# Kernel optimization log

Hardware: AMD Instinct MI355X
Metric: run time of the kernel (lower is better)

Reference implementation:

```python
import jax, jax.numpy as jnp
import numpy as np

NUM_GROUPS = 8
K = 2


def setup_inputs() -> dict:
    key = jax.random.key(0)
    k1, k2, k3 = jax.random.split(key, 3)
    b, l, d = 4, 4096, 2048
    g, k = NUM_GROUPS, K
    hdg = d // g  # 256
    x = jax.random.normal(k1, (b, l, d), dtype=jnp.float32)
    Wg = jax.random.normal(k2, (d, g), dtype=jnp.float32) * 0.02  # gate (no bias)
    Wm = jax.random.normal(k3, (k * hdg, k * hdg), dtype=jnp.float32) * 0.02  # inner Linear
    bm = jnp.zeros((k * hdg,), dtype=jnp.float32)
    return {"x": x, "Wg": Wg, "Wm": Wm, "bm": bm}


def reference(x, Wg, Wm, bm):
    b, l, d = x.shape
    g, k = NUM_GROUPS, K
    hdg = d // g
    # gate: softmax + topk over groups
    S = jax.nn.softmax(x @ Wg, axis=-1)            # [b, l, g]
    G, I = jax.lax.top_k(S, k)                     # [b, l, k] each
    x4 = x.reshape(b, l, g, hdg)
    # gather selected feature groups
    sel = jnp.take_along_axis(x4, I[..., None], axis=2)  # [b, l, k, hdg]
    h = (G[..., None] * sel).reshape(b, l, k * hdg)
    # inner model (Linear)
    h = h @ Wm + bm
    h = h.reshape(b, l, k, hdg)
    # scatter back into original groups
    bi = jnp.arange(b)[:, None, None]
    li = jnp.arange(l)[None, :, None]
    out = x4.at[bi, li, I].set(h)
    return out.reshape(b, l, d)
```

## Files before the change

kernel.cpp:

```cpp
#include <hip/hip_runtime.h>
#include <hip/hip_bf16.h>

#define NTOK   16384
#define DIM    2048
#define NGRP   8
#define HDG    256
#define NIN    512

typedef float f32x4 __attribute__((ext_vector_type(4)));
typedef short bf16x8 __attribute__((ext_vector_type(8)));

static __device__ __forceinline__ unsigned short f2bf(float f) {
    unsigned int u = __builtin_bit_cast(unsigned int, f);
    u = (u + 0x7fffu + ((u >> 16) & 1u)) >> 16;
    return (unsigned short)u;
}

__global__ __launch_bounds__(256) void prep_wm(const float* __restrict__ Wm,
                                               ushort* __restrict__ WmT) {
    __shared__ float tile[64][65];
    const int bk = blockIdx.x * 64;
    const int bn = blockIdx.y * 64;
    const int t = threadIdx.x;
    const int r = t >> 4;
    const int c = (t & 15) * 4;
#pragma unroll
    for (int i = 0; i < 4; i++) {
        const float4 v = *(const float4*)&Wm[(bk + r + i * 16) * 512 + bn + c];
        tile[r + i * 16][c + 0] = v.x;
        tile[r + i * 16][c + 1] = v.y;
        tile[r + i * 16][c + 2] = v.z;
        tile[r + i * 16][c + 3] = v.w;
    }
    __syncthreads();
#pragma unroll
    for (int i = 0; i < 4; i++) {
        const int n = r + i * 16;
        ushort4 o;
        o.x = f2bf(tile[c + 0][n]);
        o.y = f2bf(tile[c + 1][n]);
        o.z = f2bf(tile[c + 2][n]);
        o.w = f2bf(tile[c + 3][n]);
        *(ushort4*)&WmT[(bn + n) * 512 + bk + c] = o;
    }
}

__global__ __launch_bounds__(256) void gate_gather(
        const float* __restrict__ x, const float* __restrict__ Wg,
        float* __restrict__ out, ushort* __restrict__ hbuf,
        int* __restrict__ Isel) {
    const int t = threadIdx.x;
    const int lane = t & 63;
    const int wave = t >> 6;
    float wgr[8][8];
#pragma unroll
    for (int j = 0; j < 8; j++) {
        const float4 a = *(const float4*)&Wg[(t * 8 + j) * 8];
        const float4 b = *(const float4*)&Wg[(t * 8 + j) * 8 + 4];
        wgr[j][0] = a.x; wgr[j][1] = a.y; wgr[j][2] = a.z; wgr[j][3] = a.w;
        wgr[j][4] = b.x; wgr[j][5] = b.y; wgr[j][6] = b.z; wgr[j][7] = b.w;
    }
    __shared__ float red[8][4][8];
    const int tok0 = blockIdx.x * 8;

    const bool b0 = lane & 1;
    const bool b1 = lane & 2;
    const bool b2 = lane & 4;

#pragma unroll
    for (int tt = 0; tt < 8; tt++) {
        const int tok = tok0 + tt;
        const float4 x0 = *(const float4*)&x[tok * DIM + t * 8];
        const float4 x1 = *(const float4*)&x[tok * DIM + t * 8 + 4];
        const float xr[8] = {x0.x, x0.y, x0.z, x0.w, x1.x, x1.y, x1.z, x1.w};
        float acc[8];
#pragma unroll
        for (int g = 0; g < 8; g++) acc[g] = 0.f;
#pragma unroll
        for (int j = 0; j < 8; j++)
#pragma unroll
            for (int g = 0; g < 8; g++)
                acc[g] = fmaf(xr[j], wgr[j][g], acc[g]);
        float n_[4];
#pragma unroll
        for (int j = 0; j < 4; j++) {
            const float keep = b0 ? acc[2 * j + 1] : acc[2 * j];
            const float send = b0 ? acc[2 * j] : acc[2 * j + 1];
            n_[j] = keep + __shfl_xor(send, 1, 64);
        }
        float m_[2];
#pragma unroll
        for (int j = 0; j < 2; j++) {
            const float keep = b1 ? n_[2 * j + 1] : n_[2 * j];
            const float send = b1 ? n_[2 * j] : n_[2 * j + 1];
            m_[j] = keep + __shfl_xor(send, 2, 64);
        }
        float v;
        {
            const float keep = b2 ? m_[1] : m_[0];
            const float send = b2 ? m_[0] : m_[1];
            v = keep + __shfl_xor(send, 4, 64);
        }
        v += __shfl_xor(v, 8, 64);
        v += __shfl_xor(v, 16, 64);
        v += __shfl_xor(v, 32, 64);
        if (lane < 8) red[tt][wave][lane] = v;
    }
    __syncthreads();

    const int ll = lane & 31;
    const int tok_local = wave * 2 + (lane >> 5);
    const int tok = tok0 + tok_local;

    float v = red[tok_local][ll >> 3][ll & 7];
    v += __shfl_xor(v, 8, 64);
    v += __shfl_xor(v, 16, 64);
    float c[8];
    c[0] = v;
    c[1] = __shfl_xor(c[0], 1, 64);
    c[2] = __shfl_xor(c[0], 2, 64);
    c[3] = __shfl_xor(c[1], 2, 64);
    c[4] = __shfl_xor(c[0], 4, 64);
    c[5] = __shfl_xor(c[1], 4, 64);
    c[6] = __shfl_xor(c[2], 4, 64);
    c[7] = __shfl_xor(c[3], 4, 64);
    const int gbase = ll & 7;

    float m = c[0];
#pragma unroll
    for (int j = 1; j < 8; j++) m = fmaxf(m, c[j]);
    float sum = 0.f;
#pragma unroll
    for (int j = 0; j < 8; j++) sum += __expf(c[j] - m);
    int i0 = 8; float v0 = -3.4e38f;
#pragma unroll
    for (int j = 0; j < 8; j++) {
        const int g = gbase ^ j;
        if (c[j] > v0 || (c[j] == v0 && g < i0)) { v0 = c[j]; i0 = g; }
    }
    int i1 = 8; float v1 = -3.4e38f;
#pragma unroll
    for (int j = 0; j < 8; j++) {
        const int g = gbase ^ j;
        if (g != i0 && (c[j] > v1 || (c[j] == v1 && g < i1))) { v1 = c[j]; i1 = g; }
    }
    const float inv = 1.0f / sum;
    const float G0 = __expf(v0 - m) * inv;
    const float G1 = __expf(v1 - m) * inv;

#pragma unroll
    for (int cgrp = 0; cgrp < 8; cgrp++) {
        const float4 f0 = *(const float4*)&x[tok * DIM + cgrp * HDG + ll * 8];
        const float4 f1 = *(const float4*)&x[tok * DIM + cgrp * HDG + ll * 8 + 4];
        if (cgrp == i0 || cgrp == i1) {
            const float gv  = (cgrp == i0) ? G0 : G1;
            const int slot  = (cgrp == i0) ? 0 : 1;
            int4 pk;
            pk.x = (int)f2bf(gv * f0.x) | ((int)f2bf(gv * f0.y) << 16);
            pk.y = (int)f2bf(gv * f0.z) | ((int)f2bf(gv * f0.w) << 16);
            pk.z = (int)f2bf(gv * f1.x) | ((int)f2bf(gv * f1.y) << 16);
            pk.w = (int)f2bf(gv * f1.z) | ((int)f2bf(gv * f1.w) << 16);
            *(int4*)&hbuf[tok * NIN + slot * HDG + ll * 8] = pk;
        } else {
            *(float4*)&out[tok * DIM + cgrp * HDG + ll * 8]     = f0;
            *(float4*)&out[tok * DIM + cgrp * HDG + ll * 8 + 4] = f1;
        }
    }
    if (ll == 0) {
        int2 s2; s2.x = i0; s2.y = i1;
        *(int2*)&Isel[tok * 2] = s2;
    }
}

__global__ __launch_bounds__(256) void gemm_scatter(
        const ushort* __restrict__ h, const ushort* __restrict__ WmT,
        const float* __restrict__ bm, const int* __restrict__ Isel,
        float* __restrict__ out) {
    __shared__ ushort Hs[2][128][40];
    __shared__ ushort Ws[2][128][40];
    const int t = threadIdx.x;
    const int lane = t & 63;
    const int wave = t >> 6;
    const int wn = (wave >> 1) * 64;
    const int wt = (wave & 1) * 64;
    const int n_blk = blockIdx.x * 128;
    const int tok_blk = blockIdx.y * 128;

    const int sr = t >> 2;
    const int sc = (t & 3) * 8;

    const ushort* hp0 = &h[(tok_blk + sr) * 512 + sc];
    const ushort* hp1 = hp0 + 64 * 512;
    const ushort* wp0 = &WmT[(n_blk + sr) * 512 + sc];
    const ushort* wp1 = wp0 + 64 * 512;

    int4 rh0 = *(const int4*)hp0;
    int4 rh1 = *(const int4*)hp1;
    int4 rw0 = *(const int4*)wp0;
    int4 rw1 = *(const int4*)wp1;

    f32x4 acc[4][4];
#pragma unroll
    for (int i = 0; i < 4; i++)
#pragma unroll
        for (int j = 0; j < 4; j++)
            acc[i][j] = (f32x4){0.f, 0.f, 0.f, 0.f};

    const int fr = lane & 15;
    const int kh = (lane >> 4) * 8;

    for (int k = 0; k < 16; ++k) {
        const int b = k & 1;
        *(int4*)&Hs[b][sr][sc]      = rh0;
        *(int4*)&Hs[b][sr + 64][sc] = rh1;
        *(int4*)&Ws[b][sr][sc]      = rw0;
        *(int4*)&Ws[b][sr + 64][sc] = rw1;
        __syncthreads();
        if (k < 15) {
            const int off = (k + 1) * 32;
            rh0 = *(const int4*)(hp0 + off);
            rh1 = *(const int4*)(hp1 + off);
            rw0 = *(const int4*)(wp0 + off);
            rw1 = *(const int4*)(wp1 + off);
        }
        bf16x8 av[4], bv[4];
#pragma unroll
        for (int i = 0; i < 4; i++) av[i] = *(const bf16x8*)&Ws[b][wn + i * 16 + fr][kh];
#pragma unroll
        for (int j = 0; j < 4; j++) bv[j] = *(const bf16x8*)&Hs[b][wt + j * 16 + fr][kh];
#pragma unroll
        for (int i = 0; i < 4; i++)
#pragma unroll
            for (int j = 0; j < 4; j++)
                acc[i][j] = __builtin_amdgcn_mfma_f32_16x16x32_bf16(
                    av[i], bv[j], acc[i][j], 0, 0, 0);
    }

    const int rq = (lane >> 4) * 4;
    const int n_base = n_blk + wn;
    const int s = n_base >> 8;
    const int n_off_base = (n_base & 255) + rq;
    float4 bmv[4];
#pragma unroll
    for (int i = 0; i < 4; i++) bmv[i] = *(const float4*)&bm[n_base + i * 16 + rq];
#pragma unroll
    for (int j = 0; j < 4; j++) {
        const int tok = tok_blk + wt + j * 16 + fr;
        const int2 sel = *(const int2*)&Isel[tok * 2];
        const int grp = s ? sel.y : sel.x;
        float* op = &out[tok * DIM + grp * HDG + n_off_base];
#pragma unroll
        for (int i = 0; i < 4; i++) {
            float4 o;
            o.x = acc[i][j][0] + bmv[i].x;
            o.y = acc[i][j][1] + bmv[i].y;
            o.z = acc[i][j][2] + bmv[i].z;
            o.w = acc[i][j][3] + bmv[i].w;
            *(float4*)&op[i * 16] = o;
        }
    }
}

extern "C" void kernel_launch(void* const* d_in, const int* in_sizes, int n_in,
                              void* d_out, int out_size, void* d_ws, size_t ws_size,
                              hipStream_t stream) {
    const float* x  = (const float*)d_in[0];
    const float* Wg = (const float*)d_in[1];
    const float* Wm = (const float*)d_in[2];
    const float* bm = (const float*)d_in[3];
    float* out = (float*)d_out;

    char* ws = (char*)d_ws;
    ushort* hbuf = (ushort*)ws;
    ushort* WmT  = (ushort*)(ws + (size_t)16 * 1024 * 1024);
    int*    Isel = (int*)(ws + (size_t)16 * 1024 * 1024 + 512 * 1024);

    prep_wm<<<dim3(8, 8), 256, 0, stream>>>(Wm, WmT);
    gate_gather<<<NTOK / 8, 256, 0, stream>>>(x, Wg, out, hbuf, Isel);
    gemm_scatter<<<dim3(NIN / 128, NTOK / 128), 256, 0, stream>>>(hbuf, WmT, bm, Isel, out);
}
```

Baseline: 283.2 us.

## Keep gate inputs in registers and deepen GEMM global prefetch to two stages

gate_gather now loads each thread's x slice for all eight tokens into registers once. Those registers feed both the gate dot product and the gather/copy phase, so x is no longer read a second time from global memory. Gate weights and indices pass through shared memory with an extra barrier, and launch bounds request three blocks per SM. The GEMM fully unrolls its k loop and prefetches global tiles two iterations ahead with a three-slot register ring, which raises register pressure.

```diff
diff --git a/kernel.cpp b/kernel.cpp
--- a/kernel.cpp
+++ b/kernel.cpp
@@ -45,13 +45,25 @@
     }
 }
 
-__global__ __launch_bounds__(256) void gate_gather(
+__global__ __launch_bounds__(256, 3) void gate_gather(
         const float* __restrict__ x, const float* __restrict__ Wg,
         float* __restrict__ out, ushort* __restrict__ hbuf,
         int* __restrict__ Isel) {
     const int t = threadIdx.x;
     const int lane = t & 63;
     const int wave = t >> 6;
+    const int tok0 = blockIdx.x * 8;
+
+    __shared__ float red[8][4][8];
+    __shared__ float gateF[8][2];
+    __shared__ int   gateI[8][2];
+
+    int4 xa[16];
+#pragma unroll
+    for (int tt = 0; tt < 8; tt++) {
+        xa[2 * tt]     = *(const int4*)&x[(tok0 + tt) * DIM + t * 8];
+        xa[2 * tt + 1] = *(const int4*)&x[(tok0 + tt) * DIM + t * 8 + 4];
+    }
     float wgr[8][8];
 #pragma unroll
     for (int j = 0; j < 8; j++) {
@@ -60,19 +72,14 @@
         wgr[j][0] = a.x; wgr[j][1] = a.y; wgr[j][2] = a.z; wgr[j][3] = a.w;
         wgr[j][4] = b.x; wgr[j][5] = b.y; wgr[j][6] = b.z; wgr[j][7] = b.w;
     }
-    __shared__ float red[8][4][8];
-    const int tok0 = blockIdx.x * 8;
-
-    const bool b0 = lane & 1;
-    const bool b1 = lane & 2;
-    const bool b2 = lane & 4;
+
+    const bool s0 = lane & 1;
+    const bool s1 = lane & 2;
+    const bool s2 = lane & 4;
 
 #pragma unroll
     for (int tt = 0; tt < 8; tt++) {
-        const int tok = tok0 + tt;
-        const float4 x0 = *(const float4*)&x[tok * DIM + t * 8];
-        const float4 x1 = *(const float4*)&x[tok * DIM + t * 8 + 4];
-        const float xr[8] = {x0.x, x0.y, x0.z, x0.w, x1.x, x1.y, x1.z, x1.w};
+        const float* xr = (const float*)&xa[2 * tt];
         float acc[8];
 #pragma unroll
         for (int g = 0; g < 8; g++) acc[g] = 0.f;
@@ -84,21 +91,21 @@
         float n_[4];
 #pragma unroll
         for (int j = 0; j < 4; j++) {
-            const float keep = b0 ? acc[2 * j + 1] : acc[2 * j];
-            const float send = b0 ? acc[2 * j] : acc[2 * j + 1];
+            const float keep = s0 ? acc[2 * j + 1] : acc[2 * j];
+            const float send = s0 ? acc[2 * j] : acc[2 * j + 1];
             n_[j] = keep + __shfl_xor(send, 1, 64);
         }
         float m_[2];
 #pragma unroll
         for (int j = 0; j < 2; j++) {
-            const float keep = b1 ? n_[2 * j + 1] : n_[2 * j];
-            const float send = b1 ? n_[2 * j] : n_[2 * j + 1];
+            const float keep = s1 ? n_[2 * j + 1] : n_[2 * j];
+            const float send = s1 ? n_[2 * j] : n_[2 * j + 1];
             m_[j] = keep + __shfl_xor(send, 2, 64);
         }
         float v;
         {
-            const float keep = b2 ? m_[1] : m_[0];
-            const float send = b2 ? m_[0] : m_[1];
+            const float keep = s2 ? m_[1] : m_[0];
+            const float send = s2 ? m_[0] : m_[1];
             v = keep + __shfl_xor(send, 4, 64);
         }
         v += __shfl_xor(v, 8, 64);
@@ -108,67 +115,75 @@
     }
     __syncthreads();
 
-    const int ll = lane & 31;
-    const int tok_local = wave * 2 + (lane >> 5);
-    const int tok = tok0 + tok_local;
-
-    float v = red[tok_local][ll >> 3][ll & 7];
-    v += __shfl_xor(v, 8, 64);
-    v += __shfl_xor(v, 16, 64);
-    float c[8];
-    c[0] = v;
-    c[1] = __shfl_xor(c[0], 1, 64);
-    c[2] = __shfl_xor(c[0], 2, 64);
-    c[3] = __shfl_xor(c[1], 2, 64);
-    c[4] = __shfl_xor(c[0], 4, 64);
-    c[5] = __shfl_xor(c[1], 4, 64);
-    c[6] = __shfl_xor(c[2], 4, 64);
-    c[7] = __shfl_xor(c[3], 4, 64);
-    const int gbase = ll & 7;
-
-    float m = c[0];
-#pragma unroll
-    for (int j = 1; j < 8; j++) m = fmaxf(m, c[j]);
-    float sum = 0.f;
-#pragma unroll
-    for (int j = 0; j < 8; j++) sum += __expf(c[j] - m);
-    int i0 = 8; float v0 = -3.4e38f;
-#pragma unroll
-    for (int j = 0; j < 8; j++) {
-        const int g = gbase ^ j;
-        if (c[j] > v0 || (c[j] == v0 && g < i0)) { v0 = c[j]; i0 = g; }
-    }
-    int i1 = 8; float v1 = -3.4e38f;
-#pragma unroll
-    for (int j = 0; j < 8; j++) {
-        const int g = gbase ^ j;
-        if (g != i0 && (c[j] > v1 || (c[j] == v1 && g < i1))) { v1 = c[j]; i1 = g; }
-    }
-    const float inv = 1.0f / sum;
-    const float G0 = __expf(v0 - m) * inv;
-    const float G1 = __expf(v1 - m) * inv;
-
-#pragma unroll
-    for (int cgrp = 0; cgrp < 8; cgrp++) {
-        const float4 f0 = *(const float4*)&x[tok * DIM + cgrp * HDG + ll * 8];
-        const float4 f1 = *(const float4*)&x[tok * DIM + cgrp * HDG + ll * 8 + 4];
-        if (cgrp == i0 || cgrp == i1) {
-            const float gv  = (cgrp == i0) ? G0 : G1;
-            const int slot  = (cgrp == i0) ? 0 : 1;
+    {
+        const int ll = lane & 31;
+        const int tok_local = wave * 2 + (lane >> 5);
+
+        float v = red[tok_local][ll >> 3][ll & 7];
+        v += __shfl_xor(v, 8, 64);
+        v += __shfl_xor(v, 16, 64);
+        float c[8];
+        c[0] = v;
+        c[1] = __shfl_xor(c[0], 1, 64);
+        c[2] = __shfl_xor(c[0], 2, 64);
+        c[3] = __shfl_xor(c[1], 2, 64);
+        c[4] = __shfl_xor(c[0], 4, 64);
+        c[5] = __shfl_xor(c[1], 4, 64);
+        c[6] = __shfl_xor(c[2], 4, 64);
+        c[7] = __shfl_xor(c[3], 4, 64);
+        const int gbase = ll & 7;
+
+        float m = c[0];
+#pragma unroll
+        for (int j = 1; j < 8; j++) m = fmaxf(m, c[j]);
+        float sum = 0.f;
+#pragma unroll
+        for (int j = 0; j < 8; j++) sum += __expf(c[j] - m);
+        int i0 = 8; float v0 = -3.4e38f;
+#pragma unroll
+        for (int j = 0; j < 8; j++) {
+            const int g = gbase ^ j;
+            if (c[j] > v0 || (c[j] == v0 && g < i0)) { v0 = c[j]; i0 = g; }
+        }
+        int i1 = 8; float v1 = -3.4e38f;
+#pragma unroll
+        for (int j = 0; j < 8; j++) {
+            const int g = gbase ^ j;
+            if (g != i0 && (c[j] > v1 || (c[j] == v1 && g < i1))) { v1 = c[j]; i1 = g; }
+        }
+        const float inv = 1.0f / sum;
+        if (ll == 0) {
+            gateF[tok_local][0] = __expf(v0 - m) * inv;
+            gateF[tok_local][1] = __expf(v1 - m) * inv;
+            gateI[tok_local][0] = i0;
+            gateI[tok_local][1] = i1;
+            int2 sp; sp.x = i0; sp.y = i1;
+            *(int2*)&Isel[(tok0 + tok_local) * 2] = sp;
+        }
+    }
+    __syncthreads();
+
+    const int jg = t >> 5;
+    const int off = (t & 31) * 8;
+#pragma unroll
+    for (int tt = 0; tt < 8; tt++) {
+        const int tok = tok0 + tt;
+        const int i0 = gateI[tt][0];
+        const int i1 = gateI[tt][1];
+        const float* xr = (const float*)&xa[2 * tt];
+        if (jg == i0 || jg == i1) {
+            const float gv  = (jg == i0) ? gateF[tt][0] : gateF[tt][1];
+            const int slot  = (jg == i0) ? 0 : 1;
             int4 pk;
-            pk.x = (int)f2bf(gv * f0.x) | ((int)f2bf(gv * f0.y) << 16);
-            pk.y = (int)f2bf(gv * f0.z) | ((int)f2bf(gv * f0.w) << 16);
-            pk.z = (int)f2bf(gv * f1.x) | ((int)f2bf(gv * f1.y) << 16);
-            pk.w = (int)f2bf(gv * f1.z) | ((int)f2bf(gv * f1.w) << 16);
-            *(int4*)&hbuf[tok * NIN + slot * HDG + ll * 8] = pk;
+            pk.x = (int)f2bf(gv * xr[0]) | ((int)f2bf(gv * xr[1]) << 16);
+            pk.y = (int)f2bf(gv * xr[2]) | ((int)f2bf(gv * xr[3]) << 16);
+            pk.z = (int)f2bf(gv * xr[4]) | ((int)f2bf(gv * xr[5]) << 16);
+            pk.w = (int)f2bf(gv * xr[6]) | ((int)f2bf(gv * xr[7]) << 16);
+            *(int4*)&hbuf[tok * NIN + slot * HDG + off] = pk;
         } else {
-            *(float4*)&out[tok * DIM + cgrp * HDG + ll * 8]     = f0;
-            *(float4*)&out[tok * DIM + cgrp * HDG + ll * 8 + 4] = f1;
-        }
-    }
-    if (ll == 0) {
-        int2 s2; s2.x = i0; s2.y = i1;
-        *(int2*)&Isel[tok * 2] = s2;
+            *(float4*)&out[tok * DIM + t * 8]     = *(const float4*)&xr[0];
+            *(float4*)&out[tok * DIM + t * 8 + 4] = *(const float4*)&xr[4];
+        }
     }
 }
 
@@ -194,10 +209,15 @@
     const ushort* wp0 = &WmT[(n_blk + sr) * 512 + sc];
     const ushort* wp1 = wp0 + 64 * 512;
 
-    int4 rh0 = *(const int4*)hp0;
-    int4 rh1 = *(const int4*)hp1;
-    int4 rw0 = *(const int4*)wp0;
-    int4 rw1 = *(const int4*)wp1;
+    int4 rh0[3], rh1[3], rw0[3], rw1[3];
+#pragma unroll
+    for (int p = 0; p < 2; p++) {
+        const int off = p * 32;
+        rh0[p] = *(const int4*)(hp0 + off);
+        rh1[p] = *(const int4*)(hp1 + off);
+        rw0[p] = *(const int4*)(wp0 + off);
+        rw1[p] = *(const int4*)(wp1 + off);
+    }
 
     f32x4 acc[4][4];
 #pragma unroll
@@ -209,19 +229,22 @@
     const int fr = lane & 15;
     const int kh = (lane >> 4) * 8;
 
+#pragma unroll
     for (int k = 0; k < 16; ++k) {
         const int b = k & 1;
-        *(int4*)&Hs[b][sr][sc]      = rh0;
-        *(int4*)&Hs[b][sr + 64][sc] = rh1;
-        *(int4*)&Ws[b][sr][sc]      = rw0;
-        *(int4*)&Ws[b][sr + 64][sc] = rw1;
+        const int s = k % 3;
+        *(int4*)&Hs[b][sr][sc]      = rh0[s];
+        *(int4*)&Hs[b][sr + 64][sc] = rh1[s];
+        *(int4*)&Ws[b][sr][sc]      = rw0[s];
+        *(int4*)&Ws[b][sr + 64][sc] = rw1[s];
         __syncthreads();
-        if (k < 15) {
-            const int off = (k + 1) * 32;
-            rh0 = *(const int4*)(hp0 + off);
-            rh1 = *(const int4*)(hp1 + off);
-            rw0 = *(const int4*)(wp0 + off);
-            rw1 = *(const int4*)(wp1 + off);
+        if (k + 2 < 16) {
+            const int s2 = (k + 2) % 3;
+            const int off = (k + 2) * 32;
+            rh0[s2] = *(const int4*)(hp0 + off);
+            rh1[s2] = *(const int4*)(hp1 + off);
+            rw0[s2] = *(const int4*)(wp0 + off);
+            rw1[s2] = *(const int4*)(wp1 + off);
         }
         bf16x8 av[4], bv[4];
 #pragma unroll
```

Result: slower. 303.7 us (+7.2%).
